# Kernel tuning notes

Measured on AMD Instinct MI355X. Metric: run time of the kernel, lower is better.

The kernel has to match this reference:

```python
import jax, jax.numpy as jnp
import numpy as np
import math

INPUT_DIM = 1024
HIDDEN_DIM = 1024
NUM_HEADS = 16
NUM_KEYS = 4096
BATCH = 1024
BETA = 8.0


def setup_inputs() -> dict:
    key = jax.random.key(0)
    kx, kk, kv = jax.random.split(key, 3)
    bound_k = 1.0 / math.sqrt(INPUT_DIM)
    bound_v = 1.0 / math.sqrt(HIDDEN_DIM)
    x = jax.random.normal(kx, (BATCH, INPUT_DIM), dtype=jnp.float32)
    keys = jax.random.uniform(kk, (NUM_KEYS * NUM_HEADS, INPUT_DIM), dtype=jnp.float32,
                              minval=-bound_k, maxval=bound_k)
    values = jax.random.uniform(kv, (NUM_KEYS * NUM_HEADS, HIDDEN_DIM), dtype=jnp.float32,
                                minval=-bound_v, maxval=bound_v)
    return {"x": x, "keys": keys, "values": values}


def reference(x, keys, values):
    scale = math.sqrt(INPUT_DIM)
    b = x.shape[0]
    # [B, num_keys*num_heads]
    weights = (x @ keys.T) / scale
    # view as [B, num_keys, num_heads]; softmax over num_keys per head
    weights = weights.reshape(b, NUM_KEYS, NUM_HEADS)
    probs = jax.nn.softmax(BETA * weights, axis=1)
    probs = probs.reshape(b, NUM_KEYS * NUM_HEADS)
    # value retrieval
    out = probs @ values  # [B, hidden_dim]
    return out
```

## Files before the change

### kernel.cpp

```cpp
#include <hip/hip_runtime.h>
#include <hip/hip_bf16.h>
#include <stdint.h>

#define BATCH  1024
#define DIM    1024
#define NKH    65536
#define HID    1024

#define SC1 0.36067376022224085f

typedef __bf16 bf16x8 __attribute__((ext_vector_type(8)));
typedef float  f32x4  __attribute__((ext_vector_type(4)));

__device__ __forceinline__ unsigned short f2bf(float f) {
  union { float f; unsigned int u; } v; v.f = f;
  unsigned int r = v.u + 0x7fffu + ((v.u >> 16) & 1u);
  return (unsigned short)(r >> 16);
}
__device__ __forceinline__ float bf2f(unsigned short s) {
  union { unsigned int u; float f; } v; v.u = ((unsigned int)s) << 16;
  return v.f;
}
__device__ __forceinline__ unsigned int pk2(float lo, float hi) {
  union { __hip_bfloat162 h; unsigned int u; } v;
  v.h = __float22bfloat162_rn(make_float2(lo, hi));
  return v.u;
}
__device__ __forceinline__ void gl2lds16(const void* g, void* l) {
  __builtin_amdgcn_global_load_lds(
      (const __attribute__((address_space(1))) void*)g,
      (__attribute__((address_space(3))) void*)l, 16, 0, 0);
}

__global__ __launch_bounds__(256) void k_cast(
    const float* __restrict__ s, unsigned short* __restrict__ d, int n8) {
  int i = blockIdx.x * 256 + threadIdx.x;
  if (i >= n8) return;
  float4 a = ((const float4*)s)[(size_t)i * 2];
  float4 b = ((const float4*)s)[(size_t)i * 2 + 1];
  uint4 o;
  o.x = pk2(a.x, a.y); o.y = pk2(a.z, a.w);
  o.z = pk2(b.x, b.y); o.w = pk2(b.z, b.w);
  ((uint4*)d)[i] = o;
}

__global__ __launch_bounds__(256) void k_transpose_cast(
    const float* __restrict__ V, unsigned short* __restrict__ vT) {
  __shared__ float tile[64][65];
  const int t = threadIdx.x;
  const int nk0 = blockIdx.x * 64;
  const int j0  = blockIdx.y * 64;
  #pragma unroll
  for (int i = 0; i < 4; ++i) {
    int idx = t + i * 256;
    int row = idx >> 4, c4 = (idx & 15) << 2;
    float4 v = *(const float4*)(V + (size_t)(nk0 + row) * HID + (j0 + c4));
    tile[row][c4 + 0] = v.x; tile[row][c4 + 1] = v.y;
    tile[row][c4 + 2] = v.z; tile[row][c4 + 3] = v.w;
  }
  __syncthreads();
  const int q = t & 7, jj = t >> 3;
  #pragma unroll
  for (int i = 0; i < 2; ++i) {
    int j = jj + i * 32;
    uint4 o;
    o.x = pk2(tile[q*8+0][j], tile[q*8+1][j]);
    o.y = pk2(tile[q*8+2][j], tile[q*8+3][j]);
    o.z = pk2(tile[q*8+4][j], tile[q*8+5][j]);
    o.w = pk2(tile[q*8+6][j], tile[q*8+7][j]);
    *(uint4*)(vT + (size_t)(j0 + j) * NKH + (nk0 + q*8)) = o;
  }
}

__global__ __launch_bounds__(256) void k_gemm1_exp(
    const unsigned short* __restrict__ Xb, const unsigned short* __restrict__ Kb,
    unsigned short* __restrict__ E) {
  __shared__ __align__(16) unsigned short As[128 * 32];
  __shared__ __align__(16) unsigned short Bs[128 * 32];
  const int t = threadIdx.x;
  const int bm = blockIdx.x & 7, bn = blockIdx.x >> 3;
  const int m0 = bm << 7, n0 = bn << 7;
  const int lane = t & 63, wave = t >> 6;
  const int wm = (wave >> 1) << 6, wn = (wave & 1) << 6;
  const int r16 = lane & 15, quad = lane >> 4;
  const int srow = lane >> 2, kseg = (lane & 3) * 8;
  const int c0 = wave * 2, c1 = wave * 2 + 1;
  const unsigned short* gA0 = Xb + (size_t)(m0 + c0*16 + srow) * DIM + kseg;
  const unsigned short* gA1 = Xb + (size_t)(m0 + c1*16 + srow) * DIM + kseg;
  const unsigned short* gB0 = Kb + (size_t)(n0 + c0*16 + srow) * DIM + kseg;
  const unsigned short* gB1 = Kb + (size_t)(n0 + c1*16 + srow) * DIM + kseg;
  f32x4 acc[4][4] = {};
  for (int ks = 0; ks < DIM; ks += 32) {
    __syncthreads();
    gl2lds16(gA0 + ks, As + c0 * 512);
    gl2lds16(gA1 + ks, As + c1 * 512);
    gl2lds16(gB0 + ks, Bs + c0 * 512);
    gl2lds16(gB1 + ks, Bs + c1 * 512);
    __syncthreads();
    bf16x8 af[4], bfr[4];
    #pragma unroll
    for (int mi = 0; mi < 4; ++mi)
      af[mi] = *(const bf16x8*)(As + (wm + mi*16 + r16) * 32 + quad * 8);
    #pragma unroll
    for (int ni = 0; ni < 4; ++ni)
      bfr[ni] = *(const bf16x8*)(Bs + (wn + ni*16 + r16) * 32 + quad * 8);
    #pragma unroll
    for (int mi = 0; mi < 4; ++mi)
      #pragma unroll
      for (int ni = 0; ni < 4; ++ni)
        acc[mi][ni] = __builtin_amdgcn_mfma_f32_16x16x32_bf16(af[mi], bfr[ni], acc[mi][ni], 0, 0, 0);
  }
  #pragma unroll
  for (int mi = 0; mi < 4; ++mi) {
    #pragma unroll
    for (int ni = 0; ni < 4; ++ni) {
      #pragma unroll
      for (int v = 0; v < 4; ++v) {
        int row = m0 + wm + mi*16 + quad*4 + v;
        int col = n0 + wn + ni*16 + r16;
        E[(size_t)row * NKH + col] = f2bf(exp2f(acc[mi][ni][v] * SC1));
      }
    }
  }
}

__global__ __launch_bounds__(256) void k_row_denom(
    const unsigned short* __restrict__ E, float* __restrict__ r) {
  __shared__ float acc16[16];
  const int t = threadIdx.x, b = blockIdx.x;
  if (t < 16) acc16[t] = 0.0f;
  __syncthreads();
  float s0=0,s1=0,s2=0,s3=0,s4=0,s5=0,s6=0,s7=0;
  const unsigned short* row = E + (size_t)b * NKH;
  for (int c = t; c < NKH / 8; c += 256) {
    uint4 u = *(const uint4*)(row + c * 8);
    s0 += bf2f((unsigned short)(u.x & 0xffff)); s1 += bf2f((unsigned short)(u.x >> 16));
    s2 += bf2f((unsigned short)(u.y & 0xffff)); s3 += bf2f((unsigned short)(u.y >> 16));
    s4 += bf2f((unsigned short)(u.z & 0xffff)); s5 += bf2f((unsigned short)(u.z >> 16));
    s6 += bf2f((unsigned short)(u.w & 0xffff)); s7 += bf2f((unsigned short)(u.w >> 16));
  }
  const int h0 = (t & 1) * 8;
  atomicAdd(&acc16[h0 + 0], s0); atomicAdd(&acc16[h0 + 1], s1);
  atomicAdd(&acc16[h0 + 2], s2); atomicAdd(&acc16[h0 + 3], s3);
  atomicAdd(&acc16[h0 + 4], s4); atomicAdd(&acc16[h0 + 5], s5);
  atomicAdd(&acc16[h0 + 6], s6); atomicAdd(&acc16[h0 + 7], s7);
  __syncthreads();
  if (t < 16) r[b * 16 + t] = 1.0f / acc16[t];
}

__global__ __launch_bounds__(256) void k_scale(
    unsigned short* __restrict__ E, const float* __restrict__ r) {
  const int t = threadIdx.x, b = blockIdx.x;
  const int h0 = (t & 1) * 8;
  float rr[8];
  #pragma unroll
  for (int i = 0; i < 8; ++i) rr[i] = r[b * 16 + h0 + i];
  unsigned short* row = E + (size_t)b * NKH;
  for (int c = t; c < NKH / 8; c += 256) {
    uint4 u = *(uint4*)(row + c * 8);
    uint4 o;
    o.x = pk2(bf2f((unsigned short)(u.x & 0xffff)) * rr[0],
              bf2f((unsigned short)(u.x >> 16))    * rr[1]);
    o.y = pk2(bf2f((unsigned short)(u.y & 0xffff)) * rr[2],
              bf2f((unsigned short)(u.y >> 16))    * rr[3]);
    o.z = pk2(bf2f((unsigned short)(u.z & 0xffff)) * rr[4],
              bf2f((unsigned short)(u.z >> 16))    * rr[5]);
    o.w = pk2(bf2f((unsigned short)(u.w & 0xffff)) * rr[6],
              bf2f((unsigned short)(u.w >> 16))    * rr[7]);
    *(uint4*)(row + c * 8) = o;
  }
}

__global__ __launch_bounds__(256) void k_gemm2(
    const unsigned short* __restrict__ P, const unsigned short* __restrict__ Vt,
    float* __restrict__ out) {
  __shared__ __align__(16) unsigned short As[128 * 32];
  __shared__ __align__(16) unsigned short Bs[128 * 32];
  const int t = threadIdx.x;
  const int bm = blockIdx.x & 7, bn = (blockIdx.x >> 3) & 7, sp = blockIdx.x >> 6;
  const int m0 = bm << 7, n0 = bn << 7;
  const size_t kb = (size_t)sp * (NKH / 16);
  const int lane = t & 63, wave = t >> 6;
  const int wm = (wave >> 1) << 6, wn = (wave & 1) << 6;
  const int r16 = lane & 15, quad = lane >> 4;
  const int srow = lane >> 2, kseg = (lane & 3) * 8;
  const int c0 = wave * 2, c1 = wave * 2 + 1;
  const unsigned short* gA0 = P  + (size_t)(m0 + c0*16 + srow) * NKH + kb + kseg;
  const unsigned short* gA1 = P  + (size_t)(m0 + c1*16 + srow) * NKH + kb + kseg;
  const unsigned short* gB0 = Vt + (size_t)(n0 + c0*16 + srow) * NKH + kb + kseg;
  const unsigned short* gB1 = Vt + (size_t)(n0 + c1*16 + srow) * NKH + kb + kseg;
  f32x4 acc[4][4] = {};
  for (int ks = 0; ks < NKH / 16; ks += 32) {
    __syncthreads();
    gl2lds16(gA0 + ks, As + c0 * 512);
    gl2lds16(gA1 + ks, As + c1 * 512);
    gl2lds16(gB0 + ks, Bs + c0 * 512);
    gl2lds16(gB1 + ks, Bs + c1 * 512);
    __syncthreads();
    bf16x8 af[4], bfr[4];
    #pragma unroll
    for (int mi = 0; mi < 4; ++mi)
      af[mi] = *(const bf16x8*)(As + (wm + mi*16 + r16) * 32 + quad * 8);
    #pragma unroll
    for (int ni = 0; ni < 4; ++ni)
      bfr[ni] = *(const bf16x8*)(Bs + (wn + ni*16 + r16) * 32 + quad * 8);
    #pragma unroll
    for (int mi = 0; mi < 4; ++mi)
      #pragma unroll
      for (int ni = 0; ni < 4; ++ni)
        acc[mi][ni] = __builtin_amdgcn_mfma_f32_16x16x32_bf16(af[mi], bfr[ni], acc[mi][ni], 0, 0, 0);
  }
  #pragma unroll
  for (int mi = 0; mi < 4; ++mi) {
    #pragma unroll
    for (int ni = 0; ni < 4; ++ni) {
      #pragma unroll
      for (int v = 0; v < 4; ++v) {
        int row = m0 + wm + mi*16 + quad*4 + v;
        int col = n0 + wn + ni*16 + r16;
        unsafeAtomicAdd(&out[(size_t)row * HID + col], acc[mi][ni][v]);
      }
    }
  }
}

extern "C" void kernel_launch(void* const* d_in, const int* in_sizes, int n_in,
                              void* d_out, int out_size, void* d_ws, size_t ws_size,
                              hipStream_t stream) {
  (void)in_sizes; (void)n_in; (void)out_size; (void)ws_size;
  const float* x      = (const float*)d_in[0];
  const float* keys   = (const float*)d_in[1];
  const float* values = (const float*)d_in[2];
  float* out = (float*)d_out;

  unsigned short* E  = (unsigned short*)d_ws;
  unsigned short* B2 = E + (size_t)BATCH * NKH;
  unsigned short* Xb = B2 + (size_t)NKH * DIM;
  float* r = (float*)(Xb + (size_t)BATCH * DIM);

  hipMemsetAsync(d_out, 0, (size_t)BATCH * HID * sizeof(float), stream);
  k_cast<<<(NKH * (DIM / 8) + 255) / 256, 256, 0, stream>>>(keys, B2, NKH * (DIM / 8));
  k_cast<<<(BATCH * (DIM / 8) + 255) / 256, 256, 0, stream>>>(x, Xb, BATCH * (DIM / 8));
  k_gemm1_exp<<<(BATCH / 128) * (NKH / 128), 256, 0, stream>>>(Xb, B2, E);
  k_row_denom<<<BATCH, 256, 0, stream>>>(E, r);
  k_scale<<<BATCH, 256, 0, stream>>>(E, r);
  k_transpose_cast<<<dim3(NKH / 64, HID / 64), 256, 0, stream>>>(values, B2);
  k_gemm2<<<(BATCH / 128) * (HID / 128) * 16, 256, 0, stream>>>(E, B2, out);
}
```

Measured before the change: 1.138 ms.

## Store probabilities and values in K-panel layout for contiguous GEMM2 tile loads

Changes the intermediate E matrix and the transposed values buffer from row-major [rows, NKH] to panels of 32 K-columns, where each panel stores all rows contiguously with 64-byte rows. GEMM2's per-iteration tile loads become contiguous 8KB chunks instead of rows strided by 128KB, which should improve DRAM and TLB locality. The row-denominator and scale kernels are rewritten for the new layout, adding a global atomic reduction, an extra memset and a reciprocal kernel. GEMM1's epilogue now writes scattered 2-byte stores into panels.

```diff
diff --git a/kernel.cpp b/kernel.cpp
--- a/kernel.cpp
+++ b/kernel.cpp
@@ -6,6 +6,7 @@
 #define DIM    1024
 #define NKH    65536
 #define HID    1024
+#define PSTR   32768
 
 #define SC1 0.36067376022224085f
 
@@ -45,7 +46,7 @@
 }
 
 __global__ __launch_bounds__(256) void k_transpose_cast(
-    const float* __restrict__ V, unsigned short* __restrict__ vT) {
+    const float* __restrict__ V, unsigned short* __restrict__ Vb) {
   __shared__ float tile[64][65];
   const int t = threadIdx.x;
   const int nk0 = blockIdx.x * 64;
@@ -60,6 +61,8 @@
   }
   __syncthreads();
   const int q = t & 7, jj = t >> 3;
+  const int panel = (nk0 >> 5) + (q >> 2);
+  const int slot  = (q & 3) * 8;
   #pragma unroll
   for (int i = 0; i < 2; ++i) {
     int j = jj + i * 32;
@@ -68,7 +71,7 @@
     o.y = pk2(tile[q*8+2][j], tile[q*8+3][j]);
     o.z = pk2(tile[q*8+4][j], tile[q*8+5][j]);
     o.w = pk2(tile[q*8+6][j], tile[q*8+7][j]);
-    *(uint4*)(vT + (size_t)(j0 + j) * NKH + (nk0 + q*8)) = o;
+    *(uint4*)(Vb + (size_t)panel * PSTR + (size_t)(j0 + j) * 32 + slot) = o;
   }
 }
 
@@ -118,84 +121,106 @@
       for (int v = 0; v < 4; ++v) {
         int row = m0 + wm + mi*16 + quad*4 + v;
         int col = n0 + wn + ni*16 + r16;
-        E[(size_t)row * NKH + col] = f2bf(exp2f(acc[mi][ni][v] * SC1));
+        E[(size_t)(col >> 5) * PSTR + (size_t)row * 32 + (col & 31)] =
+            f2bf(exp2f(acc[mi][ni][v] * SC1));
       }
     }
   }
 }
 
 __global__ __launch_bounds__(256) void k_row_denom(
-    const unsigned short* __restrict__ E, float* __restrict__ r) {
-  __shared__ float acc16[16];
-  const int t = threadIdx.x, b = blockIdx.x;
-  if (t < 16) acc16[t] = 0.0f;
+    const unsigned short* __restrict__ E, float* __restrict__ r_acc) {
+  __shared__ float acc[64][16];
+  const int t = threadIdx.x;
+  const int b0 = (blockIdx.x & 15) * 64;
+  const int p0 = (blockIdx.x >> 4) * 128;
+  for (int i = t; i < 1024; i += 256) ((float*)acc)[i] = 0.0f;
+  const int rloc = t >> 2;
+  const int kk0  = (t & 3) * 8;
+  const int hb   = (t & 1) * 8;
+  const unsigned short* base = E + (size_t)(b0 + rloc) * 32 + kk0;
+  float s[8] = {};
+  for (int p = 0; p < 128; ++p) {
+    uint4 u = *(const uint4*)(base + (size_t)(p0 + p) * PSTR);
+    s[0] += bf2f((unsigned short)(u.x & 0xffff)); s[1] += bf2f((unsigned short)(u.x >> 16));
+    s[2] += bf2f((unsigned short)(u.y & 0xffff)); s[3] += bf2f((unsigned short)(u.y >> 16));
+    s[4] += bf2f((unsigned short)(u.z & 0xffff)); s[5] += bf2f((unsigned short)(u.z >> 16));
+    s[6] += bf2f((unsigned short)(u.w & 0xffff)); s[7] += bf2f((unsigned short)(u.w >> 16));
+  }
   __syncthreads();
-  float s0=0,s1=0,s2=0,s3=0,s4=0,s5=0,s6=0,s7=0;
-  const unsigned short* row = E + (size_t)b * NKH;
-  for (int c = t; c < NKH / 8; c += 256) {
-    uint4 u = *(const uint4*)(row + c * 8);
-    s0 += bf2f((unsigned short)(u.x & 0xffff)); s1 += bf2f((unsigned short)(u.x >> 16));
-    s2 += bf2f((unsigned short)(u.y & 0xffff)); s3 += bf2f((unsigned short)(u.y >> 16));
-    s4 += bf2f((unsigned short)(u.z & 0xffff)); s5 += bf2f((unsigned short)(u.z >> 16));
-    s6 += bf2f((unsigned short)(u.w & 0xffff)); s7 += bf2f((unsigned short)(u.w >> 16));
-  }
-  const int h0 = (t & 1) * 8;
-  atomicAdd(&acc16[h0 + 0], s0); atomicAdd(&acc16[h0 + 1], s1);
-  atomicAdd(&acc16[h0 + 2], s2); atomicAdd(&acc16[h0 + 3], s3);
-  atomicAdd(&acc16[h0 + 4], s4); atomicAdd(&acc16[h0 + 5], s5);
-  atomicAdd(&acc16[h0 + 6], s6); atomicAdd(&acc16[h0 + 7], s7);
+  #pragma unroll
+  for (int j = 0; j < 8; ++j) atomicAdd(&acc[rloc][hb + j], s[j]);
   __syncthreads();
-  if (t < 16) r[b * 16 + t] = 1.0f / acc16[t];
+  for (int i = t; i < 1024; i += 256) {
+    int rl = i >> 4, h = i & 15;
+    atomicAdd(&r_acc[(b0 + rl) * 16 + h], acc[rl][h]);
+  }
+}
+
+__global__ __launch_bounds__(256) void k_recip(
+    const float* __restrict__ r_acc, float* __restrict__ r) {
+  int i = blockIdx.x * 256 + threadIdx.x;
+  r[i] = 1.0f / r_acc[i];
 }
 
 __global__ __launch_bounds__(256) void k_scale(
     unsigned short* __restrict__ E, const float* __restrict__ r) {
-  const int t = threadIdx.x, b = blockIdx.x;
-  const int h0 = (t & 1) * 8;
-  float rr[8];
-  #pragma unroll
-  for (int i = 0; i < 8; ++i) rr[i] = r[b * 16 + h0 + i];
-  unsigned short* row = E + (size_t)b * NKH;
-  for (int c = t; c < NKH / 8; c += 256) {
-    uint4 u = *(uint4*)(row + c * 8);
-    uint4 o;
-    o.x = pk2(bf2f((unsigned short)(u.x & 0xffff)) * rr[0],
-              bf2f((unsigned short)(u.x >> 16))    * rr[1]);
-    o.y = pk2(bf2f((unsigned short)(u.y & 0xffff)) * rr[2],
-              bf2f((unsigned short)(u.y >> 16))    * rr[3]);
-    o.z = pk2(bf2f((unsigned short)(u.z & 0xffff)) * rr[4],
-              bf2f((unsigned short)(u.z >> 16))    * rr[5]);
-    o.w = pk2(bf2f((unsigned short)(u.w & 0xffff)) * rr[6],
-              bf2f((unsigned short)(u.w >> 16))    * rr[7]);
-    *(uint4*)(row + c * 8) = o;
+  const int t = threadIdx.x;
+  unsigned short* panel = E + (size_t)blockIdx.x * PSTR;
+  #pragma unroll
+  for (int i = 0; i < 4; ++i) {
+    int row = i * 256 + t;
+    const float4* rp = (const float4*)(r + row * 16);
+    float4 r0 = rp[0], r1 = rp[1], r2 = rp[2], r3 = rp[3];
+    uint4* dp = (uint4*)(panel + (size_t)row * 32);
+    uint4 u0 = dp[0], u1 = dp[1], u2 = dp[2], u3 = dp[3];
+    uint4 o0, o1, o2, o3;
+    o0.x = pk2(bf2f((unsigned short)(u0.x & 0xffff)) * r0.x, bf2f((unsigned short)(u0.x >> 16)) * r0.y);
+    o0.y = pk2(bf2f((unsigned short)(u0.y & 0xffff)) * r0.z, bf2f((unsigned short)(u0.y >> 16)) * r0.w);
+    o0.z = pk2(bf2f((unsigned short)(u0.z & 0xffff)) * r1.x, bf2f((unsigned short)(u0.z >> 16)) * r1.y);
+    o0.w = pk2(bf2f((unsigned short)(u0.w & 0xffff)) * r1.z, bf2f((unsigned short)(u0.w >> 16)) * r1.w);
+    o1.x = pk2(bf2f((unsigned short)(u1.x & 0xffff)) * r2.x, bf2f((unsigned short)(u1.x >> 16)) * r2.y);
+    o1.y = pk2(bf2f((unsigned short)(u1.y & 0xffff)) * r2.z, bf2f((unsigned short)(u1.y >> 16)) * r2.w);
+    o1.z = pk2(bf2f((unsigned short)(u1.z & 0xffff)) * r3.x, bf2f((unsigned short)(u1.z >> 16)) * r3.y);
+    o1.w = pk2(bf2f((unsigned short)(u1.w & 0xffff)) * r3.z, bf2f((unsigned short)(u1.w >> 16)) * r3.w);
+    o2.x = pk2(bf2f((unsigned short)(u2.x & 0xffff)) * r0.x, bf2f((unsigned short)(u2.x >> 16)) * r0.y);
+    o2.y = pk2(bf2f((unsigned short)(u2.y & 0xffff)) * r0.z, bf2f((unsigned short)(u2.y >> 16)) * r0.w);
+    o2.z = pk2(bf2f((unsigned short)(u2.z & 0xffff)) * r1.x, bf2f((unsigned short)(u2.z >> 16)) * r1.y);
+    o2.w = pk2(bf2f((unsigned short)(u2.w & 0xffff)) * r1.z, bf2f((unsigned short)(u2.w >> 16)) * r1.w);
+    o3.x = pk2(bf2f((unsigned short)(u3.x & 0xffff)) * r2.x, bf2f((unsigned short)(u3.x >> 16)) * r2.y);
+    o3.y = pk2(bf2f((unsigned short)(u3.y & 0xffff)) * r2.z, bf2f((unsigned short)(u3.y >> 16)) * r2.w);
+    o3.z = pk2(bf2f((unsigned short)(u3.z & 0xffff)) * r3.x, bf2f((unsigned short)(u3.z >> 16)) * r3.y);
+    o3.w = pk2(bf2f((unsigned short)(u3.w & 0xffff)) * r3.z, bf2f((unsigned short)(u3.w >> 16)) * r3.w);
+    dp[0] = o0; dp[1] = o1; dp[2] = o2; dp[3] = o3;
   }
 }
 
 __global__ __launch_bounds__(256) void k_gemm2(
-    const unsigned short* __restrict__ P, const unsigned short* __restrict__ Vt,
+    const unsigned short* __restrict__ P, const unsigned short* __restrict__ Vb,
     float* __restrict__ out) {
   __shared__ __align__(16) unsigned short As[128 * 32];
   __shared__ __align__(16) unsigned short Bs[128 * 32];
   const int t = threadIdx.x;
   const int bm = blockIdx.x & 7, bn = (blockIdx.x >> 3) & 7, sp = blockIdx.x >> 6;
   const int m0 = bm << 7, n0 = bn << 7;
-  const size_t kb = (size_t)sp * (NKH / 16);
   const int lane = t & 63, wave = t >> 6;
   const int wm = (wave >> 1) << 6, wn = (wave & 1) << 6;
   const int r16 = lane & 15, quad = lane >> 4;
   const int srow = lane >> 2, kseg = (lane & 3) * 8;
   const int c0 = wave * 2, c1 = wave * 2 + 1;
-  const unsigned short* gA0 = P  + (size_t)(m0 + c0*16 + srow) * NKH + kb + kseg;
-  const unsigned short* gA1 = P  + (size_t)(m0 + c1*16 + srow) * NKH + kb + kseg;
-  const unsigned short* gB0 = Vt + (size_t)(n0 + c0*16 + srow) * NKH + kb + kseg;
-  const unsigned short* gB1 = Vt + (size_t)(n0 + c1*16 + srow) * NKH + kb + kseg;
+  const size_t pbase = (size_t)sp * 128 * PSTR;
+  const unsigned short* gA0 = P  + pbase + (size_t)(m0 + c0*16 + srow) * 32 + kseg;
+  const unsigned short* gA1 = P  + pbase + (size_t)(m0 + c1*16 + srow) * 32 + kseg;
+  const unsigned short* gB0 = Vb + pbase + (size_t)(n0 + c0*16 + srow) * 32 + kseg;
+  const unsigned short* gB1 = Vb + pbase + (size_t)(n0 + c1*16 + srow) * 32 + kseg;
   f32x4 acc[4][4] = {};
-  for (int ks = 0; ks < NKH / 16; ks += 32) {
-    __syncthreads();
-    gl2lds16(gA0 + ks, As + c0 * 512);
-    gl2lds16(gA1 + ks, As + c1 * 512);
-    gl2lds16(gB0 + ks, Bs + c0 * 512);
-    gl2lds16(gB1 + ks, Bs + c1 * 512);
+  for (int it = 0; it < 128; ++it) {
+    const size_t off = (size_t)it * PSTR;
+    __syncthreads();
+    gl2lds16(gA0 + off, As + c0 * 512);
+    gl2lds16(gA1 + off, As + c1 * 512);
+    gl2lds16(gB0 + off, Bs + c0 * 512);
+    gl2lds16(gB1 + off, Bs + c1 * 512);
     __syncthreads();
     bf16x8 af[4], bfr[4];
     #pragma unroll
@@ -236,14 +261,17 @@
   unsigned short* E  = (unsigned short*)d_ws;
   unsigned short* B2 = E + (size_t)BATCH * NKH;
   unsigned short* Xb = B2 + (size_t)NKH * DIM;
-  float* r = (float*)(Xb + (size_t)BATCH * DIM);
+  float* r_acc = (float*)(Xb + (size_t)BATCH * DIM);
+  float* r     = r_acc + BATCH * 16;
 
   hipMemsetAsync(d_out, 0, (size_t)BATCH * HID * sizeof(float), stream);
+  hipMemsetAsync(r_acc, 0, BATCH * 16 * sizeof(float), stream);
   k_cast<<<(NKH * (DIM / 8) + 255) / 256, 256, 0, stream>>>(keys, B2, NKH * (DIM / 8));
   k_cast<<<(BATCH * (DIM / 8) + 255) / 256, 256, 0, stream>>>(x, Xb, BATCH * (DIM / 8));
   k_gemm1_exp<<<(BATCH / 128) * (NKH / 128), 256, 0, stream>>>(Xb, B2, E);
-  k_row_denom<<<BATCH, 256, 0, stream>>>(E, r);
-  k_scale<<<BATCH, 256, 0, stream>>>(E, r);
+  k_row_denom<<<256, 256, 0, stream>>>(E, r_acc);
+  k_recip<<<BATCH * 16 / 256, 256, 0, stream>>>(r_acc, r);
+  k_scale<<<NKH / 32, 256, 0, stream>>>(E, r);
   k_transpose_cast<<<dim3(NKH / 64, HID / 64), 256, 0, stream>>>(values, B2);
   k_gemm2<<<(BATCH / 128) * (HID / 128) * 16, 256, 0, stream>>>(E, B2, out);
 }
```

Result: no change. 1.143 ms (+0.5%).
